# Performance work log

Measured on AMD Instinct MI355X. Metric: run time of the kernel, lower is better.

The kernel has to match this reference:

```python
import jax, jax.numpy as jnp
import numpy as np

SIM_LEN = 16   # simulation_length T
N_CORES = 4    # chain of cores; ChipLatency == pipeline depth == N_CORES


def setup_inputs() -> dict:
    key = jax.random.key(0)
    kx, kw, kb = jax.random.split(key, 3)
    B, N, C = 64, 2048, N_CORES
    x = jax.random.uniform(kx, (B, N), dtype=jnp.float32)          # analog input in [0,1)
    weights = jax.random.normal(kw, (C, N, N), dtype=jnp.float32) / np.float32(np.sqrt(N))
    biases = jax.random.normal(kb, (C, N), dtype=jnp.float32) * 0.01
    thresholds = jnp.ones((C,), dtype=jnp.float32)
    return {"x": x, "weights": weights, "biases": biases, "thresholds": thresholds}


def _uniform_spikes(x, n_spk, cycle, T):
    # faithful translation of to_uniform_spikes(tensor, cycle)
    mask = (n_spk != 0) & (n_spk != T) & (cycle < T)
    n_safe = jnp.maximum(n_spk, 1.0)
    spacing = T / n_safe
    res = mask & (jnp.floor(cycle / spacing) < n_safe) & (jnp.floor(jnp.mod(cycle, spacing)) == 0)
    res = res.astype(x.dtype)
    res = jnp.where(n_spk == T, jnp.ones_like(res), res)
    # zeros_in is fed for cycles >= T
    return jnp.where(cycle < T, res, jnp.zeros_like(res))


def reference(x, weights, biases, thresholds):
    T = SIM_LEN
    C, N, _ = weights.shape
    B = x.shape[0]
    cycles = C + T                      # latency + simulation_length
    n_spk = jnp.round(x * T)            # spike counts per neuron for Uniform coding
    thr = thresholds[:, None, None]     # [C,1,1]

    def step(carry, cycle):
        memb, buffers, counts = carry   # memb/buffers: [C,B,N], counts: [B,N]
        in_spikes = _uniform_spikes(x, n_spk, cycle, T)            # [B,N]
        # gather phase: core 0 reads input spike train, core k reads core k-1's
        # previous-cycle spike buffer (axon source spans)
        signals = jnp.concatenate([in_spikes[None], buffers[:-1]], axis=0)  # [C,B,N]
        # integrate: memb += signals @ core_params (+ hardware bias)
        memb = memb + jnp.einsum('cba,can->cbn', signals, weights) + biases[:, None, :]
        # fire: thresholding_mode '<' -> spike where threshold < memb; soft reset
        spikes = (thr < memb).astype(x.dtype)
        memb = memb - spikes * thr
        # scatter phase: spikes become next-cycle buffers; output spans read last core
        counts = counts + spikes[-1]
        return (memb, spikes, counts), None

    init = (jnp.zeros((C, B, N), x.dtype),
            jnp.zeros((C, B, N), x.dtype),
            jnp.zeros((B, N), x.dtype))
    (_, _, counts), _ = jax.lax.scan(step, init, jnp.arange(cycles))
    return counts / T                   # rate-coded output
```

## Files before the change

kernel.cpp:

```cpp
#include <hip/hip_runtime.h>
#include <cstdint>
#include <cstddef>


#define N_DIM 2048
#define B_DIM 64
#define C_DIM 4
#define T_SIM 16
#define CYCLES 20
#define M_ROWS (CYCLES * B_DIM)

using i32x4 = __attribute__((ext_vector_type(4))) int;
using u32x4 = __attribute__((ext_vector_type(4))) uint32_t;

static constexpr size_t WQ_CORE    = (size_t)128 * 32 * 4 * 1024;
static constexpr size_t SIG_OFF    = (size_t)C_DIM * WQ_CORE;
static constexpr size_t AMAT_BYTES = (size_t)M_ROWS * N_DIM;

__device__ __forceinline__ size_t apk_off(int m, int k) {
    return ((size_t)((m >> 4) * 32 + (k >> 6)) << 10)
         + (size_t)((((k >> 4) & 3) << 8) + ((m & 15) << 4) + (k & 15));
}

__device__ __forceinline__ void pack_unit(const float* __restrict__ wc,
                                          signed char* __restrict__ wqc,
                                          int unit, int l) {
    int ct = unit & 127;
    int ks = unit >> 7;
    int n     = ct * 16 + (l & 15);
    int abase = ks * 64 + ((l >> 4) << 4);
    size_t blk_base = (((size_t)ct * 32 + ks) * 4) * 1024 + (size_t)l * 16;

    u32x4 d0, d1, d2, d3;
    for (int j4 = 0; j4 < 4; ++j4) {
        uint32_t w0 = 0, w1 = 0, w2 = 0, w3 = 0;
        for (int i = 0; i < 4; ++i) {
            int a = abase + j4 * 4 + i;
            float wv = wc[(size_t)a * N_DIM + n];
            long long vi = llrintf(wv * 8589934592.0f);
            int v  = (int)vi;
            int b0 = (int)(signed char)(v & 255); v = (v - b0) >> 8;
            int b1 = (int)(signed char)(v & 255); v = (v - b1) >> 8;
            int b2 = (int)(signed char)(v & 255); v = (v - b2) >> 8;
            int b3 = v;
            w0 |= (uint32_t)(uint8_t)b0 << (8 * i);
            w1 |= (uint32_t)(uint8_t)b1 << (8 * i);
            w2 |= (uint32_t)(uint8_t)b2 << (8 * i);
            w3 |= (uint32_t)(uint8_t)b3 << (8 * i);
        }
        d0[j4] = w0; d1[j4] = w1; d2[j4] = w2; d3[j4] = w3;
    }
    *(u32x4*)(wqc + blk_base)        = d0;
    *(u32x4*)(wqc + blk_base + 1024) = d1;
    *(u32x4*)(wqc + blk_base + 2048) = d2;
    *(u32x4*)(wqc + blk_base + 3072) = d3;
}

__device__ __forceinline__ int in_spike(float xv, int cycle) {
    if (cycle >= T_SIM) return 0;
    float n_spk = rintf(xv * 16.0f);
    if (n_spk == 16.0f) return 1;
    if (n_spk == 0.0f)  return 0;
    float spacing = 16.0f / n_spk;
    float cf = (float)cycle;
    float q = floorf(cf / spacing);
    float r = fmodf(cf, spacing);
    return (q < n_spk && floorf(r) == 0.0f) ? 1 : 0;
}

__device__ __forceinline__ void gen_unit(const float* __restrict__ x,
                                         signed char* __restrict__ a0, int gid) {
    int e   = gid << 2;
    int row = e >> 11;
    int b = row / 20, t = row - b * 20;
    int n0 = e & 2047;
    const float4 xv = *(const float4*)(x + (size_t)b * N_DIM + n0);
    uint32_t s = (uint32_t)in_spike(xv.x, t)
               | ((uint32_t)in_spike(xv.y, t) << 8)
               | ((uint32_t)in_spike(xv.z, t) << 16)
               | ((uint32_t)in_spike(xv.w, t) << 24);
    *(uint32_t*)(a0 + apk_off(row, n0)) = s;
}

__global__ __launch_bounds__(256) void prep0(const float* __restrict__ w,
                                             signed char* __restrict__ wq,
                                             const float* __restrict__ x,
                                             signed char* __restrict__ a0) {
    int wg = blockIdx.x, tid = threadIdx.x;
    if (wg < 1024) {
        pack_unit(w, wq, (wg << 2) | (tid >> 6), tid & 63);
    } else {
        gen_unit(x, a0, (wg - 1024) * 256 + tid);
    }
}

__global__ __launch_bounds__(256, 2) void gemm_core(
        signed char* __restrict__ wq, const signed char* __restrict__ apk,
        const float* __restrict__ wts, const float* __restrict__ biases,
        const float* __restrict__ thresholds,
        signed char* __restrict__ a_next, float* __restrict__ out, int c)
{
    __shared__ __align__(16) signed char smem[42240];
    const int wg  = blockIdx.x;
    const int tid = threadIdx.x;
    const int wv  = tid >> 6;
    const int l   = tid & 63;

    if (wg >= 512) {
        pack_unit(wts + (size_t)(c + 1) * N_DIM * N_DIM,
                  wq + (size_t)(c + 1) * WQ_CORE,
                  ((wg - 512) << 2) | wv, l);
        return;
    }

    const int e8 = wg >> 6;
    const int s  = wg & 63;

    const signed char* asrc  = apk + ((size_t)(e8 * 10) * 32) * 1024;
    const signed char* b0src = wq + ((size_t)(c * 128 + s * 2) * 32) * 4096;
    const signed char* b1src = wq + ((size_t)(c * 128 + s * 2 + 1) * 32) * 4096;

    auto STAGE = [&](int buf, int ks) {
        signed char* dst = smem + buf * 18432;
        if (wv < 2) {
#pragma unroll
            for (int r = 0; r < 5; ++r) {
                int blk = wv * 5 + r;
                __builtin_amdgcn_global_load_lds(
                    (const __attribute__((address_space(1))) uint32_t*)
                        (asrc + ((size_t)blk * 32 + ks) * 1024 + l * 16),
                    (__attribute__((address_space(3))) uint32_t*)(dst + blk * 1024),
                    16, 0, 0);
            }
        } else {
            const signed char* bs = (wv == 2) ? b0src : b1src;
#pragma unroll
            for (int p = 0; p < 4; ++p) {
                __builtin_amdgcn_global_load_lds(
                    (const __attribute__((address_space(1))) uint32_t*)
                        (bs + (size_t)ks * 4096 + p * 1024 + l * 16),
                    (__attribute__((address_space(3))) uint32_t*)
                        (dst + 10240 + (wv - 2) * 4096 + p * 1024),
                    16, 0, 0);
            }
        }
    };

    const int nc  = wv & 1;
    const int mtb = (wv >> 1) * 5;

    i32x4 acc[5][4];
#pragma unroll
    for (int j = 0; j < 5; ++j)
#pragma unroll
        for (int p = 0; p < 4; ++p) acc[j][p] = i32x4{0, 0, 0, 0};

    STAGE(0, 0);
    __syncthreads();
    int cur = 0;

    for (int ks = 0; ks < 32; ++ks) {
        if (ks < 31) STAGE(cur ^ 1, ks + 1);
        const signed char* lb = smem + cur * 18432 + (size_t)l * 16;
        i32x4 bf0 = *(const i32x4*)(lb + 10240 + nc * 4096);
        i32x4 bf1 = *(const i32x4*)(lb + 10240 + nc * 4096 + 1024);
        i32x4 bf2 = *(const i32x4*)(lb + 10240 + nc * 4096 + 2048);
        i32x4 bf3 = *(const i32x4*)(lb + 10240 + nc * 4096 + 3072);
#pragma unroll
        for (int j = 0; j < 5; ++j) {
            i32x4 af = *(const i32x4*)(lb + (mtb + j) * 1024);
            acc[j][0] = __builtin_amdgcn_mfma_i32_16x16x64_i8(af, bf0, acc[j][0], 0, 0, 0);
            acc[j][1] = __builtin_amdgcn_mfma_i32_16x16x64_i8(af, bf1, acc[j][1], 0, 0, 0);
            acc[j][2] = __builtin_amdgcn_mfma_i32_16x16x64_i8(af, bf2, acc[j][2], 0, 0, 0);
            acc[j][3] = __builtin_amdgcn_mfma_i32_16x16x64_i8(af, bf3, acc[j][3], 0, 0, 0);
        }
        __syncthreads();
        cur ^= 1;
    }

    double* scr = (double*)smem;
    const int nl = nc * 16 + (l & 15);
#pragma unroll
    for (int j = 0; j < 5; ++j) {
#pragma unroll
        for (int r = 0; r < 4; ++r) {
            int rl = (mtb + j) * 16 + ((l >> 4) << 2) + r;
            long long comb = ((long long)acc[j][3][r] << 24) + ((long long)acc[j][2][r] << 16)
                           + ((long long)acc[j][1][r] << 8)  +  (long long)acc[j][0][r];
            scr[rl * 33 + nl] = (double)comb * (1.0 / 8589934592.0);
        }
    }
    __syncthreads();

    const int b_loc = tid >> 5;
    const int n_loc = tid & 31;
    const int b = e8 * 8 + b_loc;
    const int n = (s << 5) + n_loc;
    const double bv = (double)biases[c * N_DIM + n];
    const double th = (double)thresholds[c];
    double m = 0.0;
    float cnt = 0.0f;
    if (c < 3) a_next[apk_off(b * 20, n)] = 0;
    for (int t = 0; t < CYCLES; ++t) {
        m = m + scr[(b_loc * 20 + t) * 33 + n_loc] + bv;
        bool sp = (th < m);
        if (sp) m -= th;
        if (c < 3) {
            if (t + 1 < CYCLES) a_next[apk_off(b * 20 + t + 1, n)] = sp ? 1 : 0;
        } else if (sp) {
            cnt += 1.0f;
        }
    }
    if (c == 3) out[(size_t)b * N_DIM + n] = cnt * 0.0625f;
}

extern "C" void kernel_launch(void* const* d_in, const int* in_sizes, int n_in,
                              void* d_out, int out_size, void* d_ws, size_t ws_size,
                              hipStream_t stream) {
    const float* x       = (const float*)d_in[0];
    const float* wts     = (const float*)d_in[1];
    const float* biases  = (const float*)d_in[2];
    const float* thr     = (const float*)d_in[3];
    float* out           = (float*)d_out;

    signed char* wq  = (signed char*)d_ws;
    signed char* sig = (signed char*)((char*)d_ws + SIG_OFF);

    prep0<<<dim3(3584), dim3(256), 0, stream>>>(wts, wq, x, sig);

    for (int c = 0; c < C_DIM; ++c) {
        const signed char* a_cur = sig + (size_t)c * AMAT_BYTES;
        signed char* a_nxt = (c < 3) ? (signed char*)(sig + (size_t)(c + 1) * AMAT_BYTES)
                                     : (signed char*)sig;
        int grid = (c < 3) ? 1536 : 512;
        gemm_core<<<dim3(grid), dim3(256), 0, stream>>>(wq, a_cur, wts, biases,
                                                        thr, a_nxt, out, c);
    }
}
```

Measured before the change: 107.3 us.

## Load B fragments directly to registers, shrink LDS and raise occupancy

The B (weight) operand is now loaded straight from global memory into registers per wave, prefetched one k-step ahead, instead of being staged through LDS. All four waves share the A-tile staging. LDS drops to one double-buffered A tile, so occupancy can rise to 4 workgroups per CU. Manual vmcnt waits and raw s_barrier replace __syncthreads, bias and threshold loads are hoisted before the loop, and the scratch padding is removed. The risks are redundant global B loads across waves, LDS bank conflicts in the unpadded scratch, and fragile hand-written wait counts.

```diff
diff --git a/kernel.cpp b/kernel.cpp
--- a/kernel.cpp
+++ b/kernel.cpp
@@ -16,6 +16,8 @@
 static constexpr size_t WQ_CORE    = (size_t)128 * 32 * 4 * 1024;
 static constexpr size_t SIG_OFF    = (size_t)C_DIM * WQ_CORE;
 static constexpr size_t AMAT_BYTES = (size_t)M_ROWS * N_DIM;
+
+#define WAITVM(n) asm volatile("s_waitcnt vmcnt(" #n ")" ::: "memory")
 
 __device__ __forceinline__ size_t apk_off(int m, int k) {
     return ((size_t)((m >> 4) * 32 + (k >> 6)) << 10)
@@ -94,13 +96,13 @@
     }
 }
 
-__global__ __launch_bounds__(256, 2) void gemm_core(
+__global__ __launch_bounds__(256, 4) void gemm_core(
         signed char* __restrict__ wq, const signed char* __restrict__ apk,
         const float* __restrict__ wts, const float* __restrict__ biases,
         const float* __restrict__ thresholds,
         signed char* __restrict__ a_next, float* __restrict__ out, int c)
 {
-    __shared__ __align__(16) signed char smem[42240];
+    __shared__ __align__(16) signed char smem[40960];
     const int wg  = blockIdx.x;
     const int tid = threadIdx.x;
     const int wv  = tid >> 6;
@@ -115,68 +117,76 @@
 
     const int e8 = wg >> 6;
     const int s  = wg & 63;
-
-    const signed char* asrc  = apk + ((size_t)(e8 * 10) * 32) * 1024;
-    const signed char* b0src = wq + ((size_t)(c * 128 + s * 2) * 32) * 4096;
-    const signed char* b1src = wq + ((size_t)(c * 128 + s * 2 + 1) * 32) * 4096;
+    const int nc  = wv & 1;
+    const int mtb = (wv >> 1) * 5;
+
+    const signed char* asrc = apk + ((size_t)(e8 * 10) * 32) * 1024;
+    const signed char* bsrc = wq + ((size_t)(c * 128 + s * 2 + nc) * 32) * 4096
+                            + (size_t)l * 16;
+
+    const int b_loc = tid >> 5;
+    const int n_loc = tid & 31;
+    const int b = e8 * 8 + b_loc;
+    const int n = (s << 5) + n_loc;
+    const double bv = (double)biases[c * N_DIM + n];
+    const double th = (double)thresholds[c];
+    asm volatile("" :: "v"(bv), "v"(th));
 
     auto STAGE = [&](int buf, int ks) {
-        signed char* dst = smem + buf * 18432;
-        if (wv < 2) {
-#pragma unroll
-            for (int r = 0; r < 5; ++r) {
-                int blk = wv * 5 + r;
+        signed char* dst = smem + buf * 10240;
+#pragma unroll
+        for (int r = 0; r < 3; ++r) {
+            int blk = wv * 3 + r;
+            if (blk < 10) {
                 __builtin_amdgcn_global_load_lds(
                     (const __attribute__((address_space(1))) uint32_t*)
                         (asrc + ((size_t)blk * 32 + ks) * 1024 + l * 16),
                     (__attribute__((address_space(3))) uint32_t*)(dst + blk * 1024),
                     16, 0, 0);
             }
-        } else {
-            const signed char* bs = (wv == 2) ? b0src : b1src;
-#pragma unroll
-            for (int p = 0; p < 4; ++p) {
-                __builtin_amdgcn_global_load_lds(
-                    (const __attribute__((address_space(1))) uint32_t*)
-                        (bs + (size_t)ks * 4096 + p * 1024 + l * 16),
-                    (__attribute__((address_space(3))) uint32_t*)
-                        (dst + 10240 + (wv - 2) * 4096 + p * 1024),
-                    16, 0, 0);
-            }
         }
     };
 
-    const int nc  = wv & 1;
-    const int mtb = (wv >> 1) * 5;
-
     i32x4 acc[5][4];
 #pragma unroll
     for (int j = 0; j < 5; ++j)
 #pragma unroll
         for (int p = 0; p < 4; ++p) acc[j][p] = i32x4{0, 0, 0, 0};
 
+    i32x4 bbuf[4];
     STAGE(0, 0);
-    __syncthreads();
+#pragma unroll
+    for (int p = 0; p < 4; ++p)
+        bbuf[p] = *(const i32x4*)(bsrc + p * 1024);
+    WAITVM(4);
+    __builtin_amdgcn_s_barrier();
     int cur = 0;
 
+#pragma unroll 1
     for (int ks = 0; ks < 32; ++ks) {
         if (ks < 31) STAGE(cur ^ 1, ks + 1);
-        const signed char* lb = smem + cur * 18432 + (size_t)l * 16;
-        i32x4 bf0 = *(const i32x4*)(lb + 10240 + nc * 4096);
-        i32x4 bf1 = *(const i32x4*)(lb + 10240 + nc * 4096 + 1024);
-        i32x4 bf2 = *(const i32x4*)(lb + 10240 + nc * 4096 + 2048);
-        i32x4 bf3 = *(const i32x4*)(lb + 10240 + nc * 4096 + 3072);
+        const signed char* lb = smem + cur * 10240 + (size_t)l * 16;
 #pragma unroll
         for (int j = 0; j < 5; ++j) {
             i32x4 af = *(const i32x4*)(lb + (mtb + j) * 1024);
-            acc[j][0] = __builtin_amdgcn_mfma_i32_16x16x64_i8(af, bf0, acc[j][0], 0, 0, 0);
-            acc[j][1] = __builtin_amdgcn_mfma_i32_16x16x64_i8(af, bf1, acc[j][1], 0, 0, 0);
-            acc[j][2] = __builtin_amdgcn_mfma_i32_16x16x64_i8(af, bf2, acc[j][2], 0, 0, 0);
-            acc[j][3] = __builtin_amdgcn_mfma_i32_16x16x64_i8(af, bf3, acc[j][3], 0, 0, 0);
-        }
-        __syncthreads();
+            acc[j][0] = __builtin_amdgcn_mfma_i32_16x16x64_i8(af, bbuf[0], acc[j][0], 0, 0, 0);
+            acc[j][1] = __builtin_amdgcn_mfma_i32_16x16x64_i8(af, bbuf[1], acc[j][1], 0, 0, 0);
+            acc[j][2] = __builtin_amdgcn_mfma_i32_16x16x64_i8(af, bbuf[2], acc[j][2], 0, 0, 0);
+            acc[j][3] = __builtin_amdgcn_mfma_i32_16x16x64_i8(af, bbuf[3], acc[j][3], 0, 0, 0);
+        }
+        if (ks < 31) {
+            const signed char* bk = bsrc + (size_t)(ks + 1) * 4096;
+#pragma unroll
+            for (int p = 0; p < 4; ++p)
+                bbuf[p] = *(const i32x4*)(bk + p * 1024);
+            WAITVM(4);
+        } else {
+            WAITVM(0);
+        }
+        __builtin_amdgcn_s_barrier();
         cur ^= 1;
     }
+    __syncthreads();
 
     double* scr = (double*)smem;
     const int nl = nc * 16 + (l & 15);
@@ -187,22 +197,16 @@
             int rl = (mtb + j) * 16 + ((l >> 4) << 2) + r;
             long long comb = ((long long)acc[j][3][r] << 24) + ((long long)acc[j][2][r] << 16)
                            + ((long long)acc[j][1][r] << 8)  +  (long long)acc[j][0][r];
-            scr[rl * 33 + nl] = (double)comb * (1.0 / 8589934592.0);
+            scr[rl * 32 + nl] = (double)comb * (1.0 / 8589934592.0);
         }
     }
     __syncthreads();
 
-    const int b_loc = tid >> 5;
-    const int n_loc = tid & 31;
-    const int b = e8 * 8 + b_loc;
-    const int n = (s << 5) + n_loc;
-    const double bv = (double)biases[c * N_DIM + n];
-    const double th = (double)thresholds[c];
     double m = 0.0;
     float cnt = 0.0f;
     if (c < 3) a_next[apk_off(b * 20, n)] = 0;
     for (int t = 0; t < CYCLES; ++t) {
-        m = m + scr[(b_loc * 20 + t) * 33 + n_loc] + bv;
+        m = m + scr[(b_loc * 20 + t) * 32 + n_loc] + bv;
         bool sp = (th < m);
         if (sp) m -= th;
         if (c < 3) {
```

Measured after the change: 172.4 us. 1.61x slower.
